# Kernel optimization log

Hardware: AMD Instinct MI355X
Metric: run time of the kernel (lower is better)

The kernel has to match this reference:

```python
import jax, jax.numpy as jnp
import numpy as np

ITER_N = 3  # iterNum
DIM = 256   # channel dim entering MPNCOV
# static flat indices of the upper triangle (row-major of dim*dim), as in Triuvec
_TRIU_I, _TRIU_J = np.triu_indices(DIM)
TRIU_IDX = jnp.asarray(_TRIU_I * DIM + _TRIU_J)


def setup_inputs() -> dict:
    key = jax.random.key(0)
    x = jax.random.normal(key, (256, 256, 14, 14), dtype=jnp.float32)
    return {"x": x}


def reference(x):
    B, C, H, W = x.shape
    M = H * W
    xr = x.reshape(B, C, M)
    # Covpool: y = x @ I_hat @ x^T with I_hat = (1/M)(I - (1/M) 1 1^T)
    # equivalently (1/M) * centered Gram matrix
    xc = xr - xr.mean(axis=2, keepdims=True)
    cov = jnp.einsum('bcm,bdm->bcd', xc, xc) / M  # [B, C, C]
    # Sqrtm: Newton-Schulz iteration (iSQRT-COV)
    I = jnp.eye(C, dtype=x.dtype)
    normA = jnp.trace(cov, axis1=1, axis2=2)  # = (1/3)*sum(cov * 3I)
    A = cov / normA[:, None, None]
    ZY = 0.5 * (3.0 * I - A)
    Yk = jnp.matmul(A, ZY)
    Zk = ZY
    for _ in range(ITER_N - 2):
        ZY = 0.5 * (3.0 * I - jnp.matmul(Zk, Yk))
        Yk = jnp.matmul(Yk, ZY)
        Zk = jnp.matmul(ZY, Zk)
    YZY = 0.5 * jnp.matmul(Yk, 3.0 * I - jnp.matmul(Zk, Yk))
    y = YZY * jnp.sqrt(normA)[:, None, None]
    # Triuvec: extract upper-triangular entries, [B, C*(C+1)/2]
    return y.reshape(B, C * C)[:, TRIU_IDX]
```

## Files before the change

### kernel.cpp

```cpp
#include <hip/hip_runtime.h>
#include <math.h>

#define BB 256
#define CC 256
#define MN 196
#define TRI 32896

#define MSC 32.0f
#define INV_MSC  (1.0f/32.0f)
#define INV_MSC2 (1.0f/1024.0f)

typedef _Float16 f16;
typedef f16   f16x8 __attribute__((ext_vector_type(8)));
typedef float f32x4 __attribute__((ext_vector_type(4)));
typedef unsigned u32x4 __attribute__((ext_vector_type(4)));

__device__ __forceinline__ unsigned pack_split(float v) {
    f16 h = (f16)v;
    f16 l = (f16)(v - (float)h);
    return (unsigned)__builtin_bit_cast(unsigned short, h) |
           ((unsigned)__builtin_bit_cast(unsigned short, l) << 16);
}
__device__ __forceinline__ float unpack_split(unsigned w) {
    f16 h = __builtin_bit_cast(f16, (unsigned short)(w & 0xffffu));
    f16 l = __builtin_bit_cast(f16, (unsigned short)(w >> 16));
    return (float)h + (float)l;
}
__device__ __forceinline__ f16x8 swap_pairs(f16x8 v) {
    return __builtin_shufflevector(v, v, 1, 0, 3, 2, 5, 4, 7, 6);
}
__device__ __forceinline__ void gload_lds16(const unsigned* g, const void* l) {
    __builtin_amdgcn_global_load_lds(
        (__attribute__((address_space(1))) void*)(size_t)g,
        (__attribute__((address_space(3))) void*)(unsigned)(size_t)l,
        16, 0, 0);
}

__global__ __launch_bounds__(256) void xsplit_kernel(const float* __restrict__ x,
                                                     float* __restrict__ vr,
                                                     unsigned* __restrict__ xs, int b0) {
    int wave = (blockIdx.x * 256 + threadIdx.x) >> 6;
    int lane = threadIdx.x & 63;
    int bl = wave >> 8;
    int c  = wave & 255;
    int bg = b0 + bl;
    const float* row = x + ((size_t)bg * CC + c) * MN;
    float a0 = row[lane], a1 = row[lane + 64], a2 = row[lane + 128];
    float a3 = (lane < MN - 192) ? row[lane + 192] : 0.0f;
    float s = a0 + a1 + a2 + a3;
    float q = a0 * a0 + a1 * a1 + a2 * a2 + a3 * a3;
    #pragma unroll
    for (int off = 32; off > 0; off >>= 1) {
        s += __shfl_xor(s, off, 64);
        q += __shfl_xor(q, off, 64);
    }
    float m = s * (1.0f / MN);
    if (lane == 0) vr[bg * CC + c] = q * (1.0f / MN) - m * m;
    unsigned* orow = xs + ((size_t)bl * CC + c) * 256;
    orow[lane]       = pack_split(MSC * (a0 - m));
    orow[lane + 64]  = pack_split(MSC * (a1 - m));
    orow[lane + 128] = pack_split(MSC * (a2 - m));
    orow[lane + 192] = (lane < 4) ? pack_split(MSC * (a3 - m)) : 0u;
}

__global__ __launch_bounds__(256) void norm_kernel(const float* __restrict__ vr,
                                                   float* __restrict__ inv,
                                                   float* __restrict__ snorm,
                                                   float* __restrict__ invs, int b0) {
    __shared__ float red[256];
    int b = b0 + blockIdx.x, i = threadIdx.x;
    red[i] = vr[b * CC + i];
    __syncthreads();
    for (int s = 128; s > 0; s >>= 1) {
        if (i < s) red[i] += red[i + s];
        __syncthreads();
    }
    if (i == 0) {
        float n = red[0];
        inv[b] = 1.0f / n;
        float sq = sqrtf(n);
        snorm[b] = sq;
        invs[b] = 1.0f / sq;
    }
}

template <bool FINAL>
__global__ __launch_bounds__(256) void gemm256(const unsigned* __restrict__ Ag,
                                               const unsigned* __restrict__ Bg,
                                               const unsigned* __restrict__ Eg,
                                               void* __restrict__ Cg,
                                               const float alpha0, const float beta0,
                                               const float diag_add,
                                               const float* __restrict__ Sg, int b0) {
    __shared__ __align__(16) unsigned char smem[32768];

    int bid = blockIdx.x;
    const int nwg = gridDim.x;
    if ((nwg & 7) == 0) {
        const int cpx = nwg >> 3;
        bid = (bid & 7) * cpx + (bid >> 3);
    }
    const int bl = bid >> 4;
    const int t  = bid & 15;
    const int ti = t >> 2, tj = t & 3;
    if (FINAL && ti > tj) return;
    const int bg = b0 + bl;
    const int tid  = threadIdx.x;
    const int lane = tid & 63;
    const int wid  = tid >> 6;
    const int wr = wid >> 1, wc = wid & 1;
    const int h = lane >> 4;
    const int d = lane & 15;

    const unsigned* Abase = Ag + (size_t)bl * (CC * CC) + (size_t)(ti * 64) * 256;
    const unsigned* Bbase = Bg + (size_t)bl * (CC * CC) + (size_t)(tj * 64) * 256;

    const unsigned* gpan = (wid < 2) ? Abase : Bbase;
    const int lbank = (wid < 2) ? 0 : 16384;
    const int rbase = (wid & 1) * 32;
    const int sr = lane >> 3;
    const int sg = (lane & 7) ^ sr;
    const unsigned* gsl = gpan + (size_t)(rbase + sr) * 256 + (sg << 2);

    auto STAGE = [&](int nb, int ks) {
        #pragma unroll
        for (int i = 0; i < 4; ++i)
            gload_lds16(gsl + (size_t)(i * 8) * 256 + ks * 32,
                        smem + lbank + nb * 8192 + (rbase + i * 8) * 128);
    };

    f32x4 acc[2][2];
    #pragma unroll
    for (int i = 0; i < 2; ++i)
        #pragma unroll
        for (int j = 0; j < 2; ++j) acc[i][j] = 0.0f;

    STAGE(0, 0);
    __syncthreads();
    #pragma unroll 1
    for (int ks = 0; ks < 8; ++ks) {
        const int nb = ks & 1;
        if (ks < 7) STAGE(nb ^ 1, ks + 1);
        const char* base = (const char*)smem + nb * 8192;
        #pragma unroll
        for (int kk = 0; kk < 2; ++kk) {
            const int swz = ((kk * 4 + h) ^ (d & 7)) << 4;
            f16x8 av[2], bv[2], bw[2];
            #pragma unroll
            for (int ib = 0; ib < 2; ++ib)
                av[ib] = *(const f16x8*)(base + (wr * 32 + ib * 16 + d) * 128 + swz);
            #pragma unroll
            for (int jb = 0; jb < 2; ++jb) {
                bv[jb] = *(const f16x8*)(base + 16384 + (wc * 32 + jb * 16 + d) * 128 + swz);
                bw[jb] = swap_pairs(bv[jb]);
            }
            #pragma unroll
            for (int ib = 0; ib < 2; ++ib)
                #pragma unroll
                for (int jb = 0; jb < 2; ++jb) {
                    acc[ib][jb] = __builtin_amdgcn_mfma_f32_16x16x32_f16(av[ib], bv[jb], acc[ib][jb], 0, 0, 0);
                    acc[ib][jb] = __builtin_amdgcn_mfma_f32_16x16x32_f16(av[ib], bw[jb], acc[ib][jb], 0, 0, 0);
                }
        }
        __syncthreads();
    }

    const int li0 = wr * 32 + h * 4;
    const int lj0 = wc * 32 + d;
    const int gi0 = ti * 64 + li0;
    const int gj0 = tj * 64 + lj0;
    unsigned* tile = (unsigned*)smem;

    if (!FINAL) {
        const float sc = (Sg != nullptr) ? Sg[bg] : 1.0f;
        const float al = alpha0 * sc;
        const float be = beta0 * sc;
        unsigned* Cb = (unsigned*)Cg + (size_t)bl * CC * CC;
        const unsigned* Eb = (Eg != nullptr) ? Eg + (size_t)bl * CC * CC : nullptr;

        if (Eb) {
            #pragma unroll
            for (int it = 0; it < 4; ++it) {
                int f = it * 256 + tid;
                int r = f >> 4, c4 = f & 15;
                *(u32x4*)&tile[r * 64 + c4 * 4] =
                    *(const u32x4*)&Eb[(size_t)(ti * 64 + r) * CC + tj * 64 + c4 * 4];
            }
        }
        __syncthreads();
        #pragma unroll
        for (int ib = 0; ib < 2; ++ib)
            #pragma unroll
            for (int jb = 0; jb < 2; ++jb)
                #pragma unroll
                for (int q = 0; q < 4; ++q) {
                    int lr = li0 + ib * 16 + q;
                    int lc = lj0 + jb * 16;
                    float val = al * acc[ib][jb][q];
                    if (Eb) val += be * unpack_split(tile[lr * 64 + lc]);
                    if (gi0 + ib * 16 + q == gj0 + jb * 16) val += diag_add;
                    tile[lr * 64 + lc] = pack_split(val);
                }
        __syncthreads();
        #pragma unroll
        for (int it = 0; it < 4; ++it) {
            int f = it * 256 + tid;
            int r = f >> 4, c4 = f & 15;
            *(u32x4*)&Cb[(size_t)(ti * 64 + r) * CC + tj * 64 + c4 * 4] =
                *(const u32x4*)&tile[r * 64 + c4 * 4];
        }
    } else {
        float* ob = (float*)Cg + (size_t)bg * TRI;
        #pragma unroll
        for (int ib = 0; ib < 2; ++ib)
            #pragma unroll
            for (int jb = 0; jb < 2; ++jb) {
                int gib = gi0 + ib * 16;
                int gj  = gj0 + jb * 16;
                #pragma unroll
                for (int q = 0; q < 4; ++q) {
                    int gi = gib + q;
                    if (gj >= gi)
                        ob[gi * CC - (gi * (gi - 1)) / 2 - gi + gj] = acc[ib][jb][q] * INV_MSC2;
                }
            }
    }
}

extern "C" void kernel_launch(void* const* d_in, const int* in_sizes, int n_in,
                              void* d_out, int out_size, void* d_ws, size_t ws_size,
                              hipStream_t stream) {
    const float* x = (const float*)d_in[0];
    float* out = (float*)d_out;
    unsigned* ws = (unsigned*)d_ws;

    const int SCR = BB * CC + 3 * BB;
    float* vr    = out + (out_size - SCR);
    float* inv   = vr + BB * CC;
    float* snorm = inv + BB;
    float* invs  = snorm + BB;

    size_t per_b = 4ull * CC * CC * sizeof(unsigned);
    int gmax = (int)(ws_size / per_b);
    int g = 1;
    while (g * 2 <= gmax && g * 2 <= BB) g *= 2;

    size_t slotf = (size_t)g * CC * CC;
    unsigned* s0 = ws;
    unsigned* s1 = ws + slotf;
    unsigned* s2 = ws + 2 * slotf;
    unsigned* s3 = ws + 3 * slotf;

    for (int b0 = 0; b0 < BB; b0 += g) {
        xsplit_kernel<<<g * 64, 256, 0, stream>>>(x, vr, s1, b0);
        norm_kernel<<<g, 256, 0, stream>>>(vr, inv, snorm, invs, b0);
        gemm256<false><<<g * 16, 256, 0, stream>>>(s1, s1, nullptr, (void*)s0,
                                                   1.0f / (MSC * MN), 0.0f, 0.0f, inv, b0);
        gemm256<false><<<g * 16, 256, 0, stream>>>(s0, s0, s0, (void*)s1, -0.5f * INV_MSC, 1.5f, 0.0f, nullptr, b0);
        gemm256<false><<<g * 16, 256, 0, stream>>>(s0, s1, s1, (void*)s2, 0.25f * INV_MSC, -0.75f, 1.5f * MSC, nullptr, b0);
        gemm256<false><<<g * 16, 256, 0, stream>>>(s1, s2, nullptr, (void*)s3, INV_MSC, 0.0f, 0.0f, snorm, b0);
        gemm256<false><<<g * 16, 256, 0, stream>>>(s2, s0, s2, (void*)s1, -0.5f * INV_MSC, 1.5f, 0.0f, invs, b0);
        gemm256<false><<<g * 16, 256, 0, stream>>>(s1, s3, nullptr, (void*)s0, -0.5f * INV_MSC, 0.0f, 1.5f * MSC, nullptr, b0);
        gemm256<true><<<g * 16, 256, 0, stream>>>(s3, s0, nullptr, d_out, 0.0f, 0.0f, 0.0f, nullptr, b0);
    }
}
```

Measured before the change: 425.0 us.

## Triple-buffer GEMM K-loop with explicit vmcnt waits and barriers

Replaces the double-buffered LDS staging in the 256x256 batched GEMM with a three-stage ring buffer (48KB LDS). Two k-slices are prefetched ahead, and the next prefetch is issued only after the current slice's LDS reads have completed. Explicit s_waitcnt vmcnt and raw s_barrier calls replace __syncthreads, so outstanding global->LDS loads can overlap the MFMA work. The larger LDS footprint may reduce occupancy, and the hand-placed waits depend on the exact count of in-flight loads to stay correct.

```diff
diff --git a/kernel.cpp b/kernel.cpp
--- a/kernel.cpp
+++ b/kernel.cpp
@@ -14,6 +14,12 @@
 typedef f16   f16x8 __attribute__((ext_vector_type(8)));
 typedef float f32x4 __attribute__((ext_vector_type(4)));
 typedef unsigned u32x4 __attribute__((ext_vector_type(4)));
+
+#define WAITVM4  asm volatile("s_waitcnt vmcnt(4)" ::: "memory")
+#define WAITVM0  asm volatile("s_waitcnt vmcnt(0)" ::: "memory")
+#define WAITLGKM asm volatile("s_waitcnt lgkmcnt(0)" ::: "memory")
+#define SCHEDB   __builtin_amdgcn_sched_barrier(0)
+#define BARRIER  __builtin_amdgcn_s_barrier()
 
 __device__ __forceinline__ unsigned pack_split(float v) {
     f16 h = (f16)v;
@@ -92,7 +98,7 @@
                                                const float alpha0, const float beta0,
                                                const float diag_add,
                                                const float* __restrict__ Sg, int b0) {
-    __shared__ __align__(16) unsigned char smem[32768];
+    __shared__ __align__(16) unsigned char smem[49152];
 
     int bid = blockIdx.x;
     const int nwg = gridDim.x;
@@ -116,17 +122,17 @@
     const unsigned* Bbase = Bg + (size_t)bl * (CC * CC) + (size_t)(tj * 64) * 256;
 
     const unsigned* gpan = (wid < 2) ? Abase : Bbase;
-    const int lbank = (wid < 2) ? 0 : 16384;
+    const int lbank = (wid < 2) ? 0 : 8192;
     const int rbase = (wid & 1) * 32;
     const int sr = lane >> 3;
     const int sg = (lane & 7) ^ sr;
     const unsigned* gsl = gpan + (size_t)(rbase + sr) * 256 + (sg << 2);
 
-    auto STAGE = [&](int nb, int ks) {
+    auto STAGE = [&](int buf, int ks) {
         #pragma unroll
         for (int i = 0; i < 4; ++i)
             gload_lds16(gsl + (size_t)(i * 8) * 256 + ks * 32,
-                        smem + lbank + nb * 8192 + (rbase + i * 8) * 128);
+                        smem + buf * 16384 + lbank + (rbase + i * 8) * 128);
     };
 
     f32x4 acc[2][2];
@@ -136,33 +142,45 @@
         for (int j = 0; j < 2; ++j) acc[i][j] = 0.0f;
 
     STAGE(0, 0);
-    __syncthreads();
-    #pragma unroll 1
+    STAGE(1, 1);
+    WAITVM4;
+    BARRIER;
+    SCHEDB;
+
+    #pragma unroll
     for (int ks = 0; ks < 8; ++ks) {
-        const int nb = ks & 1;
-        if (ks < 7) STAGE(nb ^ 1, ks + 1);
-        const char* base = (const char*)smem + nb * 8192;
+        const int buf = ks % 3;
+        const char* base = (const char*)smem + buf * 16384;
+        f16x8 av[2][2], bv[2][2];
         #pragma unroll
         for (int kk = 0; kk < 2; ++kk) {
             const int swz = ((kk * 4 + h) ^ (d & 7)) << 4;
-            f16x8 av[2], bv[2], bw[2];
             #pragma unroll
             for (int ib = 0; ib < 2; ++ib)
-                av[ib] = *(const f16x8*)(base + (wr * 32 + ib * 16 + d) * 128 + swz);
-            #pragma unroll
-            for (int jb = 0; jb < 2; ++jb) {
-                bv[jb] = *(const f16x8*)(base + 16384 + (wc * 32 + jb * 16 + d) * 128 + swz);
-                bw[jb] = swap_pairs(bv[jb]);
+                av[kk][ib] = *(const f16x8*)(base + (wr * 32 + ib * 16 + d) * 128 + swz);
+            #pragma unroll
+            for (int jb = 0; jb < 2; ++jb)
+                bv[kk][jb] = *(const f16x8*)(base + 8192 + (wc * 32 + jb * 16 + d) * 128 + swz);
+        }
+        WAITLGKM;
+        SCHEDB;
+        if (ks + 2 < 8) STAGE((ks + 2) % 3, ks + 2);
+        #pragma unroll
+        for (int kk = 0; kk < 2; ++kk) {
+            f16x8 bw0 = swap_pairs(bv[kk][0]);
+            f16x8 bw1 = swap_pairs(bv[kk][1]);
+            #pragma unroll
+            for (int ib = 0; ib < 2; ++ib) {
+                acc[ib][0] = __builtin_amdgcn_mfma_f32_16x16x32_f16(av[kk][ib], bv[kk][0], acc[ib][0], 0, 0, 0);
+                acc[ib][0] = __builtin_amdgcn_mfma_f32_16x16x32_f16(av[kk][ib], bw0,       acc[ib][0], 0, 0, 0);
+                acc[ib][1] = __builtin_amdgcn_mfma_f32_16x16x32_f16(av[kk][ib], bv[kk][1], acc[ib][1], 0, 0, 0);
+                acc[ib][1] = __builtin_amdgcn_mfma_f32_16x16x32_f16(av[kk][ib], bw1,       acc[ib][1], 0, 0, 0);
             }
-            #pragma unroll
-            for (int ib = 0; ib < 2; ++ib)
-                #pragma unroll
-                for (int jb = 0; jb < 2; ++jb) {
-                    acc[ib][jb] = __builtin_amdgcn_mfma_f32_16x16x32_f16(av[ib], bv[jb], acc[ib][jb], 0, 0, 0);
-                    acc[ib][jb] = __builtin_amdgcn_mfma_f32_16x16x32_f16(av[ib], bw[jb], acc[ib][jb], 0, 0, 0);
-                }
-        }
-        __syncthreads();
+        }
+        SCHEDB;
+        if (ks < 6) { WAITVM4; } else { WAITVM0; }
+        BARRIER;
+        SCHEDB;
     }
 
     const int li0 = wr * 32 + h * 4;
```

After: 400.3 us. 1.06x faster.
